# Performance work log

Hardware: AMD Instinct MI355X
Metric: run time of the kernel (lower is better)

## Reference

```python
import jax, jax.numpy as jnp
import numpy as np

N = 20000        # nodes
E = 320000       # edges (avg degree 16)
F_IN = 256       # n_feat
HID = 64         # n_hid (per-head channels, layer 1)
HEADS = 8        # hard-coded n_head in GAT2
NCLS = 64        # n_classes
NEG_SLOPE = 0.2  # PyG GATv2Conv default leaky_relu slope
EPS = 1e-16      # PyG softmax denominator epsilon


def setup_inputs() -> dict:
    key = jax.random.key(0)
    ks = jax.random.split(key, 10)
    glorot = lambda k, shape: jax.random.normal(k, shape, jnp.float32) * (1.0 / np.sqrt(shape[0]))
    return {
        "x": jax.random.normal(ks[0], (N, F_IN), jnp.float32),
        "edge_index": jax.random.randint(ks[1], (2, E), 0, N, dtype=jnp.int32),
        # layer 1: GATv2Conv(F_IN -> HID, heads=HEADS, concat=True)
        "Wl1": glorot(ks[2], (F_IN, HEADS * HID)),
        "Wr1": glorot(ks[3], (F_IN, HEADS * HID)),
        "att1": glorot(ks[4], (HEADS, HID)),
        "b1": jnp.zeros((HEADS * HID,), jnp.float32),
        # layer 2: GATv2Conv(HEADS*HID -> NCLS, heads=1, concat=False)
        "Wl2": glorot(ks[5], (HEADS * HID, NCLS)),
        "Wr2": glorot(ks[6], (HEADS * HID, NCLS)),
        "att2": glorot(ks[7], (1, NCLS)),
        "b2": jnp.zeros((NCLS,), jnp.float32),
    }


def gatv2_layer(x, Wl, Wr, att, bias, src, dst, heads, concat):
    # x: [N, Fin]; Wl/Wr: [Fin, heads*C]; att: [heads, C]
    n = x.shape[0]
    c = att.shape[1]
    xl = (x @ Wl).reshape(n, heads, c)   # source-side projection
    xr = (x @ Wr).reshape(n, heads, c)   # target-side projection
    # per-edge GATv2 score: a^T leaky_relu(Wl x_j + Wr x_i)
    e = jax.nn.leaky_relu(xl[src] + xr[dst], NEG_SLOPE)      # [E, H, C]
    alpha = jnp.einsum('ehc,hc->eh', e, att)                 # [E, H]
    # segment softmax over incoming edges of each target node
    amax = jax.ops.segment_max(alpha, dst, num_segments=n)   # [N, H]
    amax = jnp.where(jnp.isfinite(amax), amax, 0.0)
    ex = jnp.exp(alpha - amax[dst])
    denom = jax.ops.segment_sum(ex, dst, num_segments=n)     # [N, H]
    w = ex / (denom[dst] + EPS)                              # [E, H]
    # weighted scatter-aggregate of source features
    out = jax.ops.segment_sum(xl[src] * w[:, :, None], dst, num_segments=n)  # [N, H, C]
    out = out.reshape(n, heads * c) if concat else out.mean(axis=1)
    return out + bias


def reference(x, edge_index, Wl1, Wr1, att1, b1, Wl2, Wr2, att2, b2):
    src, dst = edge_index[0], edge_index[1]
    h = gatv2_layer(x, Wl1, Wr1, att1, b1, src, dst, HEADS, True)   # [N, 512]
    h = jax.nn.elu(h)
    out = gatv2_layer(h, Wl2, Wr2, att2, b2, src, dst, 1, False)    # [N, 64]
    return out
```

## Files before the change

### kernel.cpp

```cpp
#include <hip/hip_runtime.h>
#include <hip/hip_bf16.h>

#define N_NODES 20000
#define N_EDGES 320000
#define F_IN 256
#define HID 64
#define HEADS 8
#define NCLS 64
#define D1 (HEADS * HID)
#define SCAN_BLOCKS ((N_NODES + 255) / 256)

typedef __attribute__((ext_vector_type(8))) short short8;
typedef __attribute__((ext_vector_type(4))) float floatx4;
typedef __attribute__((ext_vector_type(2))) float v2f;

__device__ __forceinline__ ushort f2bf(float f) {
    unsigned u = __float_as_uint(f);
    unsigned r = (u + 0x7fffu + ((u >> 16) & 1u)) >> 16;
    return (ushort)r;
}
__device__ __forceinline__ v2f unpack2(unsigned u) {
    v2f r;
    r.x = __uint_as_float(u << 16);
    r.y = __uint_as_float(u & 0xffff0000u);
    return r;
}
template <int CTRL>
__device__ __forceinline__ float dppadd(float x) {
    int y = __builtin_amdgcn_update_dpp(0, __float_as_int(x), CTRL, 0xF, 0xF, true);
    return x + __int_as_float(y);
}
__device__ __forceinline__ float rowsum16(float x) {
    x = dppadd<0xB1>(x);
    x = dppadd<0x4E>(x);
    x = dppadd<0x124>(x);
    x = dppadd<0x128>(x);
    return x;
}
__device__ __forceinline__ void async_copy16(ushort* lds, const ushort* g) {
    __builtin_amdgcn_global_load_lds(
        (const __attribute__((address_space(1))) void*)g,
        (__attribute__((address_space(3))) void*)lds, 16, 0, 0);
}

#define PB_HIST 1250
#define PB_CONV 5000
#define PB_T1   512
#define PB_T2   128
#define PB_TOTAL (PB_HIST + PB_CONV + 2 * PB_T1 + 2 * PB_T2)
__global__ __launch_bounds__(256) void preprocess(
    const float* __restrict__ x, ushort* __restrict__ xbf,
    const float* __restrict__ Wl1, const float* __restrict__ Wr1,
    const float* __restrict__ Wl2, const float* __restrict__ Wr2,
    ushort* __restrict__ wt1, ushort* __restrict__ wt2,
    const int* __restrict__ dst, int* __restrict__ cnt) {
    int b = blockIdx.x, t = threadIdx.x;
    if (b < PB_HIST) {
        int i = b * 256 + t;
        if (i < N_EDGES) atomicAdd(&cnt[dst[i]], 1);
    } else if (b < PB_HIST + PB_CONV) {
        int i = (b - PB_HIST) * 256 + t;
        if (i < N_NODES * F_IN / 4) {
            float4 v = ((const float4*)x)[i];
            ushort4 o;
            o.x = f2bf(v.x); o.y = f2bf(v.y); o.z = f2bf(v.z); o.w = f2bf(v.w);
            ((ushort4*)xbf)[i] = o;
        }
    } else if (b < PB_HIST + PB_CONV + 2 * PB_T1) {
        int lb = b - PB_HIST - PB_CONV;
        const float* W = (lb < PB_T1) ? Wl1 : Wr1;
        ushort* Wt = wt1 + ((lb < PB_T1) ? 0 : D1 * F_IN);
        int i = (lb % PB_T1) * 256 + t;
        if (i < D1 * F_IN) {
            Wt[(i & 511) * 256 + (i >> 9)] = f2bf(W[i]);
        }
    } else {
        int lb = b - PB_HIST - PB_CONV - 2 * PB_T1;
        const float* W = (lb < PB_T2) ? Wl2 : Wr2;
        ushort* Wt = wt2 + ((lb < PB_T2) ? 0 : NCLS * D1);
        int i = (lb % PB_T2) * 256 + t;
        if (i < NCLS * D1) {
            Wt[(i & 63) * 512 + (i >> 6)] = f2bf(W[i]);
        }
    }
}

__global__ __launch_bounds__(256) void scan_local(const int* __restrict__ cnt,
                                                  int* __restrict__ pscan,
                                                  int* __restrict__ bsum, int n) {
    int tid = threadIdx.x;
    int i = blockIdx.x * 256 + tid;
    int lane = tid & 63, wave = tid >> 6;
    int v = (i < n) ? cnt[i] : 0;
    int x = v;
    #pragma unroll
    for (int d = 1; d < 64; d <<= 1) {
        int y = __shfl_up(x, d);
        if (lane >= d) x += y;
    }
    __shared__ int wsum[4];
    if (lane == 63) wsum[wave] = x;
    __syncthreads();
    int woff = 0;
    for (int w2 = 0; w2 < wave; w2++) woff += wsum[w2];
    int incl = x + woff;
    if (i < n) pscan[i] = incl;
    if (tid == 255) bsum[blockIdx.x] = incl;
}

__global__ __launch_bounds__(256) void scan_finalize(const int* __restrict__ cnt,
                                                     const int* __restrict__ pscan,
                                                     const int* __restrict__ bsum,
                                                     int* __restrict__ row_ptr,
                                                     int* __restrict__ cursor, int n) {
    int t = threadIdx.x;
    int lane = t & 63, wave = t >> 6;
    int v = (t < SCAN_BLOCKS && t < blockIdx.x) ? bsum[t] : 0;
    #pragma unroll
    for (int mask = 1; mask < 64; mask <<= 1) v += __shfl_xor(v, mask);
    __shared__ int ws[4];
    __shared__ int soff;
    if (lane == 0) ws[wave] = v;
    __syncthreads();
    if (t == 0) soff = ws[0] + ws[1] + ws[2] + ws[3];
    __syncthreads();
    int i = blockIdx.x * 256 + t;
    if (i < n) {
        int incl = pscan[i] + soff;
        row_ptr[i + 1] = incl;
        cursor[i] = incl - cnt[i];
    }
    if (i == 0) row_ptr[0] = 0;
}

#define G1_NT 8
#define G1_MT ((N_NODES + 127) / 128)
#define G1_BLOCKS (G1_NT * G1_MT)
#define SC_BLOCKS (N_EDGES / 256)
__global__ __launch_bounds__(256) void gemm1_scatter(
    const ushort* __restrict__ A, const ushort* __restrict__ Bt,
    ushort* __restrict__ C,
    const int* __restrict__ src, const int* __restrict__ dst,
    int* __restrict__ cursor, int* __restrict__ csr_src) {
    if (blockIdx.x >= G1_BLOCKS) {
        int i = (blockIdx.x - G1_BLOCKS) * 256 + threadIdx.x;
        if (i < N_EDGES) {
            int d = dst[i];
            int pos = atomicAdd(&cursor[d], 1);
            csr_src[pos] = src[i];
        }
        return;
    }
    const int M = N_NODES, N = 2 * D1, K = F_IN;
    __shared__ ushort As[128 * 32];
    __shared__ ushort Bs[128 * 32];
    int tid = threadIdx.x;
    int rowBase = (blockIdx.x >> 3) * 128, colBase = (blockIdx.x & 7) * 128;
    int wave = tid >> 6, lane = tid & 63;
    int quad = lane >> 4, m16 = lane & 15;
    int rh = wave >> 1, chf = wave & 1;
    floatx4 acc[4][4];
    #pragma unroll
    for (int i = 0; i < 4; i++)
        #pragma unroll
        for (int j = 0; j < 4; j++) acc[i][j] = (floatx4){0.f, 0.f, 0.f, 0.f};

    for (int k0 = 0; k0 < K; k0 += 32) {
        #pragma unroll
        for (int i = 0; i < 2; i++) {
            int idx = i * 256 + tid;
            int r = idx >> 2, kq = (idx & 3) * 8;
            int grow = min(rowBase + r, M - 1);
            async_copy16(&As[idx * 8], A + (size_t)grow * K + k0 + kq);
            async_copy16(&Bs[idx * 8], Bt + (size_t)(colBase + r) * K + k0 + kq);
        }
        __syncthreads();
        short8 af[4], bfr[4];
        #pragma unroll
        for (int i = 0; i < 4; i++)
            af[i] = *(short8*)&As[(rh * 64 + i * 16 + m16) * 32 + quad * 8];
        #pragma unroll
        for (int j = 0; j < 4; j++)
            bfr[j] = *(short8*)&Bs[(chf * 64 + j * 16 + m16) * 32 + quad * 8];
        #pragma unroll
        for (int i = 0; i < 4; i++)
            #pragma unroll
            for (int j = 0; j < 4; j++)
                acc[i][j] = __builtin_amdgcn_mfma_f32_16x16x32_bf16(af[i], bfr[j], acc[i][j], 0, 0, 0);
        __syncthreads();
    }
    #pragma unroll
    for (int i = 0; i < 4; i++)
        #pragma unroll
        for (int j = 0; j < 4; j++)
            #pragma unroll
            for (int r = 0; r < 4; r++) {
                int row = rowBase + rh * 64 + i * 16 + quad * 4 + r;
                if (row < M) C[(size_t)row * N + colBase + chf * 64 + j * 16 + m16] = f2bf(acc[i][j][r]);
            }
}

__global__ __launch_bounds__(256) void gemm2_32x128(
    const ushort* __restrict__ A, const ushort* __restrict__ Bt,
    ushort* __restrict__ C) {
    const int K = D1;
    __shared__ ushort As[32 * 32];
    __shared__ ushort Bs[128 * 32];
    int tid = threadIdx.x;
    int rowBase = blockIdx.x * 32;
    int wave = tid >> 6, lane = tid & 63;
    int quad = lane >> 4, m16 = lane & 15;
    floatx4 acc[2][2];
    #pragma unroll
    for (int i = 0; i < 2; i++)
        #pragma unroll
        for (int j = 0; j < 2; j++) acc[i][j] = (floatx4){0.f, 0.f, 0.f, 0.f};

    for (int k0 = 0; k0 < K; k0 += 32) {
        if (tid < 128) {
            int r = tid >> 2, kq = (tid & 3) * 8;
            async_copy16(&As[tid * 8], A + (size_t)(rowBase + r) * K + k0 + kq);
        }
        #pragma unroll
        for (int i = 0; i < 2; i++) {
            int idx = i * 256 + tid;
            int r = idx >> 2, kq = (idx & 3) * 8;
            async_copy16(&Bs[idx * 8], Bt + (size_t)r * K + k0 + kq);
        }
        __syncthreads();
        short8 af[2], bfr[2];
        #pragma unroll
        for (int i = 0; i < 2; i++)
            af[i] = *(short8*)&As[(i * 16 + m16) * 32 + quad * 8];
        #pragma unroll
        for (int j = 0; j < 2; j++)
            bfr[j] = *(short8*)&Bs[(wave * 32 + j * 16 + m16) * 32 + quad * 8];
        #pragma unroll
        for (int i = 0; i < 2; i++)
            #pragma unroll
            for (int j = 0; j < 2; j++)
                acc[i][j] = __builtin_amdgcn_mfma_f32_16x16x32_bf16(af[i], bfr[j], acc[i][j], 0, 0, 0);
        __syncthreads();
    }
    #pragma unroll
    for (int i = 0; i < 2; i++)
        #pragma unroll
        for (int j = 0; j < 2; j++)
            #pragma unroll
            for (int r = 0; r < 4; r++) {
                int row = rowBase + i * 16 + quad * 4 + r;
                C[(size_t)row * 128 + wave * 32 + j * 16 + m16] = f2bf(acc[i][j][r]);
            }
}

#define L1PROC(cu, valid)                                                     \
    {                                                                         \
        v2f _c01 = unpack2((cu).x), _c23 = unpack2((cu).y);                   \
        v2f _v01 = _c01 + xr01, _v23 = _c23 + xr23;                           \
        v2f _sp = a6_01 * _v01 + a4_01 * __builtin_elementwise_abs(_v01)      \
                + a6_23 * _v23 + a4_23 * __builtin_elementwise_abs(_v23);     \
        float _sc = _sp.x + _sp.y;                                            \
        _sc = rowsum16(_sc);                                                  \
        float _e = (valid) ? exp2f(_sc) : 0.f;                                \
        den += _e;                                                            \
        v2f _ev = {_e, _e};                                                   \
        ac01 = ac01 + _ev * _c01; ac23 = ac23 + _ev * _c23;                   \
    }

__global__ __launch_bounds__(128) void attn_l1_fused(
    const ushort* __restrict__ xlr, const float* __restrict__ att,
    const float* __restrict__ b1,
    const int* __restrict__ row_ptr, const int* __restrict__ csr_src,
    ushort* __restrict__ h1out) {
    int d = blockIdx.x, t = threadIdx.x;
    int start = row_ptr[d], deg = row_ptr[d + 1] - start;

    uint2 xru = *(const uint2*)(xlr + (size_t)d * 1024 + 512 + 4 * t);
    v2f xr01 = unpack2(xru.x), xr23 = unpack2(xru.y);
    const float C6 = 0.6f * 1.44269504f, C4 = 0.4f * 1.44269504f;
    float4 atv = *(const float4*)(att + 4 * t);
    v2f a6_01 = {C6 * atv.x, C6 * atv.y}, a4_01 = {C4 * atv.x, C4 * atv.y};
    v2f a6_23 = {C6 * atv.z, C6 * atv.w}, a4_23 = {C4 * atv.z, C4 * atv.w};

    float den = 0.f;
    v2f ac01 = {0.f, 0.f}, ac23 = {0.f, 0.f};

    if (deg > 0) {
        const int* cs = csr_src + start;
        uint2 q0 = *(const uint2*)(xlr + (size_t)cs[0] * 1024 + 4 * t);
        uint2 q1 = *(const uint2*)(xlr + (size_t)cs[min(1, deg - 1)] * 1024 + 4 * t);
        uint2 q2 = *(const uint2*)(xlr + (size_t)cs[min(2, deg - 1)] * 1024 + 4 * t);
        uint2 q3 = *(const uint2*)(xlr + (size_t)cs[min(3, deg - 1)] * 1024 + 4 * t);
        for (int i0 = 0; i0 < deg; i0 += 4) {
            uint2 e0 = q0, e1 = q1, e2 = q2, e3 = q3;
            if (i0 + 4 < deg) q0 = *(const uint2*)(xlr + (size_t)cs[i0 + 4] * 1024 + 4 * t);
            if (i0 + 5 < deg) q1 = *(const uint2*)(xlr + (size_t)cs[i0 + 5] * 1024 + 4 * t);
            if (i0 + 6 < deg) q2 = *(const uint2*)(xlr + (size_t)cs[i0 + 6] * 1024 + 4 * t);
            if (i0 + 7 < deg) q3 = *(const uint2*)(xlr + (size_t)cs[i0 + 7] * 1024 + 4 * t);
            L1PROC(e0, true)
            L1PROC(e1, i0 + 1 < deg)
            L1PROC(e2, i0 + 2 < deg)
            L1PROC(e3, i0 + 3 < deg)
        }
    }
    float inv = 1.f / (den + 1e-16f);
    float4 bv = *(const float4*)(b1 + 4 * t);
    float o0 = ac01.x * inv + bv.x;
    float o1 = ac01.y * inv + bv.y;
    float o2 = ac23.x * inv + bv.z;
    float o3 = ac23.y * inv + bv.w;
    o0 = o0 > 0.f ? o0 : (__expf(o0) - 1.f);
    o1 = o1 > 0.f ? o1 : (__expf(o1) - 1.f);
    o2 = o2 > 0.f ? o2 : (__expf(o2) - 1.f);
    o3 = o3 > 0.f ? o3 : (__expf(o3) - 1.f);
    ushort4 hv;
    hv.x = f2bf(o0); hv.y = f2bf(o1); hv.z = f2bf(o2); hv.w = f2bf(o3);
    *(ushort4*)(h1out + (size_t)d * D1 + 4 * t) = hv;
}

#define L2PROC(cu, valid)                                                     \
    {                                                                         \
        v2f _c01 = unpack2((cu).x), _c23 = unpack2((cu).y);                   \
        v2f _v01 = _c01 + yr01, _v23 = _c23 + yr23;                           \
        v2f _sp = at6_01 * _v01 + at4_01 * __builtin_elementwise_abs(_v01)    \
                + at6_23 * _v23 + at4_23 * __builtin_elementwise_abs(_v23);   \
        float _sc = _sp.x + _sp.y;                                            \
        _sc = rowsum16(_sc);                                                  \
        float _e = (valid) ? exp2f(_sc) : 0.f;                                \
        den += _e;                                                            \
        v2f _ev = {_e, _e};                                                   \
        ac01 = ac01 + _ev * _c01; ac23 = ac23 + _ev * _c23;                   \
    }

__device__ __forceinline__ float xgroup_sum(float x) {
    float t = __int_as_float(__builtin_amdgcn_ds_swizzle(__float_as_int(x), 0x401F));
    x += t;
    x += __shfl_xor(x, 32);
    return x;
}

__global__ __launch_bounds__(256) void attn_l2_fused(
    const ushort* __restrict__ ylr, const float* __restrict__ att2,
    const float* __restrict__ b2,
    const int* __restrict__ row_ptr, const int* __restrict__ csr_src,
    float* __restrict__ out) {
    int wave = threadIdx.x >> 6, lane = threadIdx.x & 63;
    int d = blockIdx.x * 4 + wave;
    int grp = lane >> 4, l15 = lane & 15;
    int start = row_ptr[d], deg = row_ptr[d + 1] - start;

    uint2 yru = *(const uint2*)(ylr + (size_t)d * 128 + 64 + 4 * l15);
    v2f yr01 = unpack2(yru.x), yr23 = unpack2(yru.y);
    float4 a2 = *(const float4*)(att2 + 4 * l15);
    const float C6 = 0.6f * 1.44269504f, C4 = 0.4f * 1.44269504f;
    v2f at6_01 = {C6 * a2.x, C6 * a2.y}, at4_01 = {C4 * a2.x, C4 * a2.y};
    v2f at6_23 = {C6 * a2.z, C6 * a2.w}, at4_23 = {C4 * a2.z, C4 * a2.w};

    float den = 0.f;
    v2f ac01 = {0.f, 0.f}, ac23 = {0.f, 0.f};

    if (deg > 0) {
        int S = (deg + 3) >> 2;
        const int* cs = csr_src + start;
        uint2 q0 = *(const uint2*)(ylr + (size_t)cs[min(grp, deg - 1)] * 128 + 4 * l15);
        uint2 q1 = *(const uint2*)(ylr + (size_t)cs[min(min(1, S - 1) * 4 + grp, deg - 1)] * 128 + 4 * l15);
        for (int i = 0; i < S; i++) {
            uint2 cu = q0;
            q0 = q1;
            if (i + 2 < S) {
                int p = min((i + 2) * 4 + grp, deg - 1);
                q1 = *(const uint2*)(ylr + (size_t)cs[p] * 128 + 4 * l15);
            }
            L2PROC(cu, 4 * i + grp < deg)
        }
        den = xgroup_sum(den);
        ac01.x = xgroup_sum(ac01.x);
        ac01.y = xgroup_sum(ac01.y);
        ac23.x = xgroup_sum(ac23.x);
        ac23.y = xgroup_sum(ac23.y);
    }
    if (grp == 0) {
        float inv = 1.f / (den + 1e-16f);
        float4 bv = *(const float4*)(b2 + 4 * l15);
        float4 o;
        o.x = ac01.x * inv + bv.x;
        o.y = ac01.y * inv + bv.y;
        o.z = ac23.x * inv + bv.z;
        o.w = ac23.y * inv + bv.w;
        *(float4*)(out + (size_t)d * NCLS + 4 * l15) = o;
    }
}

extern "C" void kernel_launch(void* const* d_in, const int* in_sizes, int n_in,
                              void* d_out, int out_size, void* d_ws, size_t ws_size,
                              hipStream_t stream) {
    const float* x    = (const float*)d_in[0];
    const int*   edge = (const int*)d_in[1];
    const float* Wl1  = (const float*)d_in[2];
    const float* Wr1  = (const float*)d_in[3];
    const float* att1 = (const float*)d_in[4];
    const float* b1   = (const float*)d_in[5];
    const float* Wl2  = (const float*)d_in[6];
    const float* Wr2  = (const float*)d_in[7];
    const float* att2 = (const float*)d_in[8];
    const float* b2   = (const float*)d_in[9];
    float* out = (float*)d_out;

    const int* srcv = edge;
    const int* dstv = edge + N_EDGES;

    ushort* xbf  = (ushort*)d_ws;
    ushort* wt1  = xbf + (size_t)N_NODES * F_IN;
    ushort* wt2  = wt1 + 2 * D1 * F_IN;
    ushort* xlr  = wt2 + 2 * NCLS * D1;
    ushort* h1   = xlr + (size_t)N_NODES * 2 * D1;
    ushort* ylr  = h1 + (size_t)N_NODES * D1;
    int* cnt     = (int*)(ylr + (size_t)N_NODES * 2 * NCLS);
    int* pscan   = cnt + N_NODES;
    int* bsum    = pscan + N_NODES;
    int* row_ptr = bsum + 128;
    int* cursor  = row_ptr + N_NODES + 1;
    int* csr_src = cursor + N_NODES;

    hipMemsetAsync(cnt, 0, N_NODES * sizeof(int), stream);
    preprocess<<<PB_TOTAL, 256, 0, stream>>>(x, xbf, Wl1, Wr1, Wl2, Wr2, wt1, wt2, dstv, cnt);
    scan_local<<<SCAN_BLOCKS, 256, 0, stream>>>(cnt, pscan, bsum, N_NODES);
    scan_finalize<<<SCAN_BLOCKS, 256, 0, stream>>>(cnt, pscan, bsum, row_ptr, cursor, N_NODES);
    gemm1_scatter<<<G1_BLOCKS + SC_BLOCKS, 256, 0, stream>>>(
        xbf, wt1, xlr, srcv, dstv, cursor, csr_src);
    attn_l1_fused<<<N_NODES, 128, 0, stream>>>(xlr, att1, b1, row_ptr, csr_src, h1);
    gemm2_32x128<<<N_NODES / 32, 256, 0, stream>>>(h1, wt2, ylr);
    attn_l2_fused<<<N_NODES / 4, 256, 0, stream>>>(ylr, att2, b2, row_ptr, csr_src, out);
}
```

Baseline: 215.7 us.

## Use k-chunk-major shared memory layout and 64-wide K steps in GEMMs

Both GEMM kernels now store shared-memory tiles k-chunk-major (8-element chunks indexed by chunk then row) instead of row-major with a 32-element stride. This is meant to remove bank conflicts on the 16-byte fragment reads feeding the MFMA instructions. The K step also doubles from 32 to 64, which halves the number of barrier pairs per tile at the cost of twice the LDS footprint. The global loads become less contiguous per row, since consecutive threads now fetch the same k chunk from different rows.

```diff
diff --git a/kernel.cpp b/kernel.cpp
--- a/kernel.cpp
+++ b/kernel.cpp
@@ -152,8 +152,8 @@
         return;
     }
     const int M = N_NODES, N = 2 * D1, K = F_IN;
-    __shared__ ushort As[128 * 32];
-    __shared__ ushort Bs[128 * 32];
+    __shared__ ushort As[8 * 128 * 8];
+    __shared__ ushort Bs[8 * 128 * 8];
     int tid = threadIdx.x;
     int rowBase = (blockIdx.x >> 3) * 128, colBase = (blockIdx.x & 7) * 128;
     int wave = tid >> 6, lane = tid & 63;
@@ -165,28 +165,31 @@
         #pragma unroll
         for (int j = 0; j < 4; j++) acc[i][j] = (floatx4){0.f, 0.f, 0.f, 0.f};
 
-    for (int k0 = 0; k0 < K; k0 += 32) {
-        #pragma unroll
-        for (int i = 0; i < 2; i++) {
+    for (int k0 = 0; k0 < K; k0 += 64) {
+        #pragma unroll
+        for (int i = 0; i < 4; i++) {
             int idx = i * 256 + tid;
-            int r = idx >> 2, kq = (idx & 3) * 8;
+            int kc = idx >> 7, r = idx & 127;
             int grow = min(rowBase + r, M - 1);
-            async_copy16(&As[idx * 8], A + (size_t)grow * K + k0 + kq);
-            async_copy16(&Bs[idx * 8], Bt + (size_t)(colBase + r) * K + k0 + kq);
+            async_copy16(&As[idx * 8], A + (size_t)grow * K + k0 + kc * 8);
+            async_copy16(&Bs[idx * 8], Bt + (size_t)(colBase + r) * K + k0 + kc * 8);
         }
         __syncthreads();
-        short8 af[4], bfr[4];
-        #pragma unroll
-        for (int i = 0; i < 4; i++)
-            af[i] = *(short8*)&As[(rh * 64 + i * 16 + m16) * 32 + quad * 8];
-        #pragma unroll
-        for (int j = 0; j < 4; j++)
-            bfr[j] = *(short8*)&Bs[(chf * 64 + j * 16 + m16) * 32 + quad * 8];
-        #pragma unroll
-        for (int i = 0; i < 4; i++)
+        #pragma unroll
+        for (int kk = 0; kk < 2; kk++) {
+            short8 af[4], bfr[4];
+            #pragma unroll
+            for (int i = 0; i < 4; i++)
+                af[i] = *(short8*)&As[((kk * 4 + quad) * 128 + rh * 64 + i * 16 + m16) * 8];
             #pragma unroll
             for (int j = 0; j < 4; j++)
-                acc[i][j] = __builtin_amdgcn_mfma_f32_16x16x32_bf16(af[i], bfr[j], acc[i][j], 0, 0, 0);
+                bfr[j] = *(short8*)&Bs[((kk * 4 + quad) * 128 + chf * 64 + j * 16 + m16) * 8];
+            #pragma unroll
+            for (int i = 0; i < 4; i++)
+                #pragma unroll
+                for (int j = 0; j < 4; j++)
+                    acc[i][j] = __builtin_amdgcn_mfma_f32_16x16x32_bf16(af[i], bfr[j], acc[i][j], 0, 0, 0);
+        }
         __syncthreads();
     }
     #pragma unroll
@@ -204,8 +207,8 @@
     const ushort* __restrict__ A, const ushort* __restrict__ Bt,
     ushort* __restrict__ C) {
     const int K = D1;
-    __shared__ ushort As[32 * 32];
-    __shared__ ushort Bs[128 * 32];
+    __shared__ ushort As[8 * 32 * 8];
+    __shared__ ushort Bs[8 * 128 * 8];
     int tid = threadIdx.x;
     int rowBase = blockIdx.x * 32;
     int wave = tid >> 6, lane = tid & 63;
@@ -216,30 +219,33 @@
         #pragma unroll
         for (int j = 0; j < 2; j++) acc[i][j] = (floatx4){0.f, 0.f, 0.f, 0.f};
 
-    for (int k0 = 0; k0 < K; k0 += 32) {
-        if (tid < 128) {
-            int r = tid >> 2, kq = (tid & 3) * 8;
-            async_copy16(&As[tid * 8], A + (size_t)(rowBase + r) * K + k0 + kq);
-        }
-        #pragma unroll
-        for (int i = 0; i < 2; i++) {
+    for (int k0 = 0; k0 < K; k0 += 64) {
+        {
+            int kc = tid >> 5, r = tid & 31;
+            async_copy16(&As[tid * 8], A + (size_t)(rowBase + r) * K + k0 + kc * 8);
+        }
+        #pragma unroll
+        for (int i = 0; i < 4; i++) {
             int idx = i * 256 + tid;
-            int r = idx >> 2, kq = (idx & 3) * 8;
-            async_copy16(&Bs[idx * 8], Bt + (size_t)r * K + k0 + kq);
+            int kc = idx >> 7, r = idx & 127;
+            async_copy16(&Bs[idx * 8], Bt + (size_t)r * K + k0 + kc * 8);
         }
         __syncthreads();
-        short8 af[2], bfr[2];
-        #pragma unroll
-        for (int i = 0; i < 2; i++)
-            af[i] = *(short8*)&As[(i * 16 + m16) * 32 + quad * 8];
-        #pragma unroll
-        for (int j = 0; j < 2; j++)
-            bfr[j] = *(short8*)&Bs[(wave * 32 + j * 16 + m16) * 32 + quad * 8];
-        #pragma unroll
-        for (int i = 0; i < 2; i++)
+        #pragma unroll
+        for (int kk = 0; kk < 2; kk++) {
+            short8 af[2], bfr[2];
+            #pragma unroll
+            for (int i = 0; i < 2; i++)
+                af[i] = *(short8*)&As[((kk * 4 + quad) * 32 + i * 16 + m16) * 8];
             #pragma unroll
             for (int j = 0; j < 2; j++)
-                acc[i][j] = __builtin_amdgcn_mfma_f32_16x16x32_bf16(af[i], bfr[j], acc[i][j], 0, 0, 0);
+                bfr[j] = *(short8*)&Bs[((kk * 4 + quad) * 128 + wave * 32 + j * 16 + m16) * 8];
+            #pragma unroll
+            for (int i = 0; i < 2; i++)
+                #pragma unroll
+                for (int j = 0; j < 2; j++)
+                    acc[i][j] = __builtin_amdgcn_mfma_f32_16x16x32_bf16(af[i], bfr[j], acc[i][j], 0, 0, 0);
+        }
         __syncthreads();
     }
     #pragma unroll
```

Result: slower. 232.0 us (+7.5%).
